# Performance work log

Measured on AMD Instinct MI355X. Metric: run time of the kernel, lower is better.

The kernel has to match this reference:

```python
import jax, jax.numpy as jnp
import numpy as np

IN_DIM = 1024
BS, NCROPS = 32, 1024


def setup_inputs() -> dict:
    key = jax.random.key(0)
    ks = jax.random.split(key, 7)
    s = 1.0 / np.sqrt(IN_DIM)
    return {
        "x": jax.random.normal(ks[0], (BS, NCROPS, IN_DIM), jnp.float32),
        "Wq": jax.random.uniform(ks[1], (IN_DIM,), jnp.float32, -s, s),
        "bq": jax.random.uniform(ks[2], (1,), jnp.float32, -s, s),
        "Wk": jax.random.uniform(ks[3], (IN_DIM,), jnp.float32, -s, s),
        "bk": jax.random.uniform(ks[4], (1,), jnp.float32, -s, s),
        "Wv": jax.random.uniform(ks[5], (IN_DIM, IN_DIM), jnp.float32, -s, s),
        "bv": jax.random.uniform(ks[6], (IN_DIM,), jnp.float32, -s, s),
    }


def reference(x, Wq, bq, Wk, bk, Wv, bv):
    # x: (bs, n, d). 1x1 Conv1d over permuted x == per-position linear maps.
    bs, n, d = x.shape
    q = jnp.einsum("bnd,d->bn", x, Wq) + bq  # (bs, n)   query_conv -> 1 channel
    k = jnp.einsum("bnd,d->bn", x, Wk) + bk  # (bs, n)   key_conv   -> 1 channel
    energy = q[:, :, None] * k[:, None, :]    # (bs, n, n) rank-1 outer product (bmm of (n,1)@(1,n))
    attention = jax.nn.softmax(energy, axis=-1)
    v = jnp.einsum("od,bnd->bon", Wv, x) + bv[None, :, None]  # (bs, d, n) value_conv
    out = jnp.einsum("bdn,bnm->bdm", v, attention)            # (bs, d, n)
    # Faithful to torch .view: raw reshape of (bs, d, n) -> (bs, n, d), NOT a transpose.
    out = out.reshape(bs, n, d)
    return (out, attention)
```

## Files before the change

### kernel.cpp

```cpp
#include <hip/hip_runtime.h>
#include <hip/hip_bf16.h>

#define BS  32
#define N   1024
#define DIM 1024

typedef unsigned short u16;
typedef unsigned int   u32;

typedef __attribute__((ext_vector_type(8))) __bf16 bf16x8;
typedef __attribute__((ext_vector_type(4))) float  f32x4;

__device__ __forceinline__ u16 f2bf(float f) {
    u32 u = __builtin_bit_cast(u32, f);
    u = (u + 0x7FFF + ((u >> 16) & 1)) >> 16;
    return (u16)u;
}

__device__ __forceinline__ void async16(const u16* g, u16* l) {
    __builtin_amdgcn_global_load_lds(
        (const __attribute__((address_space(1))) u32*)g,
        (__attribute__((address_space(3))) u32*)l,
        16, 0, 0);
}

__global__ void convert_qk(const float* __restrict__ x,
                           const float* __restrict__ Wq, const float* __restrict__ bq,
                           const float* __restrict__ Wk, const float* __restrict__ bk,
                           const float* __restrict__ Wv,
                           u16* __restrict__ xb, u16* __restrict__ Wvb,
                           float* __restrict__ qv, float* __restrict__ kv)
{
    int gw   = (blockIdx.x * 256 + threadIdx.x) >> 6;
    int lane = threadIdx.x & 63;
    bool isX = gw < BS * N;
    const float* src = isX ? (x + (size_t)gw * DIM) : (Wv + (size_t)(gw - BS * N) * DIM);
    u16*         dst = isX ? (xb + (size_t)gw * DIM) : (Wvb + (size_t)(gw - BS * N) * DIM);
    float qd = 0.f, kd = 0.f;
    #pragma unroll
    for (int i = 0; i < 4; ++i) {
        int e = i * 256 + lane * 4;
        float4 xv = *(const float4*)&src[e];
        uint2 p;
        p.x = (u32)f2bf(xv.x) | ((u32)f2bf(xv.y) << 16);
        p.y = (u32)f2bf(xv.z) | ((u32)f2bf(xv.w) << 16);
        *(uint2*)&dst[e] = p;
        if (isX) {
            float4 wq = *(const float4*)&Wq[e];
            float4 wk = *(const float4*)&Wk[e];
            qd += xv.x * wq.x + xv.y * wq.y + xv.z * wq.z + xv.w * wq.w;
            kd += xv.x * wk.x + xv.y * wk.y + xv.z * wk.z + xv.w * wk.w;
        }
    }
    if (isX) {
        #pragma unroll
        for (int off = 32; off; off >>= 1) {
            qd += __shfl_xor(qd, off);
            kd += __shfl_xor(kd, off);
        }
        if (lane == 0) { qv[gw] = qd + bq[0]; kv[gw] = kd + bk[0]; }
    }
}

__global__ void qz_writer(const float* __restrict__ qv, const float* __restrict__ kvg,
                          float2* __restrict__ qzg)
{
    int blk = blockIdx.x;
    int b   = blk >> 6;
    int r0  = (blk & 63) * 16;
    __shared__ float ks[1024];
    int tid = threadIdx.x;
    #pragma unroll
    for (int i = 0; i < 4; ++i) ks[i * 256 + tid] = kvg[b * N + i * 256 + tid];
    int row = tid >> 4;
    int c16 = tid & 15;
    float qrow = qv[b * N + r0 + row];
    __syncthreads();
    float z = 0.f;
    #pragma unroll 4
    for (int s = 0; s < 16; ++s) {
        const float4 kk = *(const float4*)&ks[(c16 + s * 16) * 4];
        z += __expf(qrow * kk.x) + __expf(qrow * kk.y)
           + __expf(qrow * kk.z) + __expf(qrow * kk.w);
    }
    z += __shfl_xor(z, 1); z += __shfl_xor(z, 2);
    z += __shfl_xor(z, 4); z += __shfl_xor(z, 8);
    if (c16 == 0) qzg[b * N + r0 + row] = make_float2(qrow, 1.0f / z);
}

__global__ void att_tiles(const float2* __restrict__ qzg, const float* __restrict__ kvg,
                          float* __restrict__ att, u16* __restrict__ attT)
{
    int blk  = blockIdx.x;
    int b    = blk >> 8;
    int rest = blk & 255;
    int r0 = (rest >> 4) * 64;
    int c0 = (rest & 15) * 64;
    int tid = threadIdx.x;
    int tx = tid & 15, ty = tid >> 4;

    float q[4], iz[4];
    #pragma unroll
    for (int i = 0; i < 4; ++i) {
        float2 p = qzg[(size_t)b * N + r0 + tx * 4 + i];
        q[i] = p.x; iz[i] = p.y;
    }
    float kvj[4];
    #pragma unroll
    for (int j = 0; j < 4; ++j) kvj[j] = kvg[(size_t)b * N + c0 + ty * 4 + j];

    float e[4][4];
    #pragma unroll
    for (int i = 0; i < 4; ++i)
        #pragma unroll
        for (int j = 0; j < 4; ++j)
            e[i][j] = __expf(q[i] * kvj[j]) * iz[i];

    float* ab = att + (size_t)b * N * N;
    #pragma unroll
    for (int i = 0; i < 4; ++i) {
        float4 o = make_float4(e[i][0], e[i][1], e[i][2], e[i][3]);
        *(float4*)&ab[(size_t)(r0 + tx * 4 + i) * N + c0 + ty * 4] = o;
    }
    u16* tb = attT + (size_t)b * N * N;
    #pragma unroll
    for (int j = 0; j < 4; ++j) {
        uint2 p;
        p.x = (u32)f2bf(e[0][j]) | ((u32)f2bf(e[1][j]) << 16);
        p.y = (u32)f2bf(e[2][j]) | ((u32)f2bf(e[3][j]) << 16);
        *(uint2*)&tb[(size_t)(c0 + ty * 4 + j) * N + r0 + tx * 4] = p;
    }
}

__global__ __launch_bounds__(256) void gemm_bt(
    const u16* __restrict__ A,
    const u16* __restrict__ B, size_t bBatch,
    u16* __restrict__ C, size_t cBatch,
    const float* __restrict__ bias)
{
    const int K = 1024, LD = 1024;
    int blk  = blockIdx.x;
    int rest = blk >> 3;
    int b    = (blk & 7) * 4 + (rest >> 6);
    int t    = rest & 63;
    int m0  = (t >> 3) * 128, n0 = (t & 7) * 128;
    const u16* Ab = A;
    const u16* Bb = B + bBatch * (size_t)b;
    __shared__ u16 lA[128 * 32];
    __shared__ u16 lB[128 * 32];
    int w = threadIdx.x >> 6, lane = threadIdx.x & 63;
    int wr = (w >> 1) * 64, wc = (w & 1) * 64;
    int rowl = lane >> 2;
    int col8 = (lane & 3) * 8;
    int frow = lane & 15, fk = (lane >> 4) * 8;
    f32x4 acc[4][4] = {};

    for (int k0 = 0; k0 < K; k0 += 32) {
        #pragma unroll
        for (int s = 0; s < 2; ++s) {
            int rr = (s * 4 + w) * 16;
            async16(Ab + (size_t)(m0 + rr + rowl) * LD + k0 + col8, &lA[rr * 32]);
            async16(Bb + (size_t)(n0 + rr + rowl) * LD + k0 + col8, &lB[rr * 32]);
        }
        __syncthreads();
        bf16x8 af[4], bfr[4];
        #pragma unroll
        for (int i = 0; i < 4; ++i)
            af[i] = *(const bf16x8*)&lA[(wr + i * 16 + frow) * 32 + fk];
        #pragma unroll
        for (int j = 0; j < 4; ++j)
            bfr[j] = *(const bf16x8*)&lB[(wc + j * 16 + frow) * 32 + fk];
        #pragma unroll
        for (int i = 0; i < 4; ++i)
            #pragma unroll
            for (int j = 0; j < 4; ++j)
                acc[i][j] = __builtin_amdgcn_mfma_f32_16x16x32_bf16(af[i], bfr[j], acc[i][j], 0, 0, 0);
        __syncthreads();
    }

    int r4 = (lane >> 4) * 4, cc = lane & 15;
    u16* Cb = C + cBatch * (size_t)b;
    #pragma unroll
    for (int i = 0; i < 4; ++i)
        #pragma unroll
        for (int j = 0; j < 4; ++j)
            #pragma unroll
            for (int rg = 0; rg < 4; ++rg) {
                int row = m0 + wr + i * 16 + r4 + rg;
                int col = n0 + wc + j * 16 + cc;
                Cb[(size_t)row * LD + col] = f2bf(acc[i][j][rg] + bias[row]);
            }
}

__global__ __launch_bounds__(256) void gemm2_bt(
    const u16* __restrict__ A, size_t aBatch,
    const u16* __restrict__ B, size_t bBatch,
    float* __restrict__ C, size_t cBatch)
{
    const int K = 1024, LD = 1024;
    int blk  = blockIdx.x;
    int rest = blk >> 3;
    int b    = (blk & 7) * 4 + (rest >> 6);
    int t    = rest & 63;
    int m0  = (t >> 3) * 128, n0 = (t & 7) * 128;
    const u16* Ab = A + aBatch * (size_t)b;
    const u16* Bb = B + bBatch * (size_t)b;
    __shared__ u16 lA[128 * 32];
    __shared__ u16 lB[128 * 32];
    int w = threadIdx.x >> 6, lane = threadIdx.x & 63;
    int wr = (w >> 1) * 64, wc = (w & 1) * 64;
    int rowl = lane >> 2;
    int col8 = (lane & 3) * 8;
    int frow = lane & 15, fk = (lane >> 4) * 8;
    f32x4 acc[4][4] = {};

    for (int k0 = 0; k0 < K; k0 += 32) {
        #pragma unroll
        for (int s = 0; s < 2; ++s) {
            int rr = (s * 4 + w) * 16;
            async16(Ab + (size_t)(m0 + rr + rowl) * LD + k0 + col8, &lA[rr * 32]);
            async16(Bb + (size_t)(n0 + rr + rowl) * LD + k0 + col8, &lB[rr * 32]);
        }
        __syncthreads();
        bf16x8 af[4], bfr[4];
        #pragma unroll
        for (int i = 0; i < 4; ++i)
            af[i] = *(const bf16x8*)&lA[(wr + i * 16 + frow) * 32 + fk];
        #pragma unroll
        for (int j = 0; j < 4; ++j)
            bfr[j] = *(const bf16x8*)&lB[(wc + j * 16 + frow) * 32 + fk];
        #pragma unroll
        for (int i = 0; i < 4; ++i)
            #pragma unroll
            for (int j = 0; j < 4; ++j)
                acc[i][j] = __builtin_amdgcn_mfma_f32_16x16x32_bf16(af[i], bfr[j], acc[i][j], 0, 0, 0);
        __syncthreads();
    }

    int r4 = (lane >> 4) * 4, cc = lane & 15;
    float* Cb = C + cBatch * (size_t)b;
    #pragma unroll
    for (int i = 0; i < 4; ++i)
        #pragma unroll
        for (int j = 0; j < 4; ++j)
            #pragma unroll
            for (int rg = 0; rg < 4; ++rg) {
                int row = m0 + wr + i * 16 + r4 + rg;
                int col = n0 + wc + j * 16 + cc;
                Cb[(size_t)row * LD + col] = acc[i][j][rg];
            }
}

extern "C" void kernel_launch(void* const* d_in, const int* in_sizes, int n_in,
                              void* d_out, int out_size, void* d_ws, size_t ws_size,
                              hipStream_t stream)
{
    const float* x  = (const float*)d_in[0];
    const float* Wq = (const float*)d_in[1];
    const float* bq = (const float*)d_in[2];
    const float* Wk = (const float*)d_in[3];
    const float* bk = (const float*)d_in[4];
    const float* Wv = (const float*)d_in[5];
    const float* bv = (const float*)d_in[6];

    float* out = (float*)d_out;
    float* att = out + (size_t)BS * N * N;

    char* ws = (char*)d_ws;
    u16*  xb   = (u16*)ws;
    u16*  vb   = xb + (size_t)BS * N * DIM;
    u16*  Wvb  = vb + (size_t)BS * N * DIM;
    float* qv  = (float*)(Wvb + (size_t)DIM * DIM);
    float* kv  = qv + BS * N;
    float2* qzg = (float2*)(kv + BS * N);
    u16*  attT = (u16*)(qzg + BS * N);

    convert_qk<<<(BS * N + DIM) / 4, 256, 0, stream>>>(x, Wq, bq, Wk, bk, Wv, xb, Wvb, qv, kv);
    qz_writer<<<BS * 64, 256, 0, stream>>>(qv, kv, qzg);
    gemm_bt<<<BS * 64, 256, 0, stream>>>(Wvb, xb, (size_t)N * DIM, vb, (size_t)N * DIM, bv);
    att_tiles<<<BS * 256, 256, 0, stream>>>(qzg, kv, att, attT);
    gemm2_bt<<<BS * 64, 256, 0, stream>>>(vb, (size_t)N * DIM, attT, (size_t)N * N, out, (size_t)N * DIM);
}
```

Measured before the change: 609.1 us.

## Replace both GEMMs with 256x256-tile, 8-wave, double-buffered swizzled-LDS MFMA kernel

The two simple 128x128 bf16 GEMM kernels, which synchronize on every K-step, are replaced by one templated kernel. It uses 256x256 output tiles, 512 threads, a 128KB double-buffered LDS ring with XOR-swizzled rows, and 64-wide K tiles. Global-to-LDS async loads are issued in quarter-tile chunks interleaved with the MFMA phases, with explicit vmcnt/lgkmcnt waits and s_setprio. The aim is to hide load latency, cut LDS bank conflicts and raise per-block arithmetic intensity. The cost is heavy register and LDS pressure (at most one block per CU with 128KB of LDS) and fragile hand-placed wait counts.

Result: faster. 524.6 us, median of 2 (-13.9%).

```diff
diff --git a/kernel.cpp b/kernel.cpp
--- a/kernel.cpp
+++ b/kernel.cpp
@@ -15,13 +15,6 @@
     u32 u = __builtin_bit_cast(u32, f);
     u = (u + 0x7FFF + ((u >> 16) & 1)) >> 16;
     return (u16)u;
-}
-
-__device__ __forceinline__ void async16(const u16* g, u16* l) {
-    __builtin_amdgcn_global_load_lds(
-        (const __attribute__((address_space(1))) u32*)g,
-        (__attribute__((address_space(3))) u32*)l,
-        16, 0, 0);
 }
 
 __global__ void convert_qk(const float* __restrict__ x,
@@ -132,123 +125,149 @@
     }
 }
 
-__global__ __launch_bounds__(256) void gemm_bt(
-    const u16* __restrict__ A,
-    const u16* __restrict__ B, size_t bBatch,
-    u16* __restrict__ C, size_t cBatch,
-    const float* __restrict__ bias)
-{
-    const int K = 1024, LD = 1024;
-    int blk  = blockIdx.x;
-    int rest = blk >> 3;
-    int b    = (blk & 7) * 4 + (rest >> 6);
-    int t    = rest & 63;
-    int m0  = (t >> 3) * 128, n0 = (t & 7) * 128;
-    const u16* Ab = A;
-    const u16* Bb = B + bBatch * (size_t)b;
-    __shared__ u16 lA[128 * 32];
-    __shared__ u16 lB[128 * 32];
-    int w = threadIdx.x >> 6, lane = threadIdx.x & 63;
-    int wr = (w >> 1) * 64, wc = (w & 1) * 64;
-    int rowl = lane >> 2;
-    int col8 = (lane & 3) * 8;
-    int frow = lane & 15, fk = (lane >> 4) * 8;
-    f32x4 acc[4][4] = {};
-
-    for (int k0 = 0; k0 < K; k0 += 32) {
-        #pragma unroll
-        for (int s = 0; s < 2; ++s) {
-            int rr = (s * 4 + w) * 16;
-            async16(Ab + (size_t)(m0 + rr + rowl) * LD + k0 + col8, &lA[rr * 32]);
-            async16(Bb + (size_t)(n0 + rr + rowl) * LD + k0 + col8, &lB[rr * 32]);
-        }
-        __syncthreads();
-        bf16x8 af[4], bfr[4];
-        #pragma unroll
-        for (int i = 0; i < 4; ++i)
-            af[i] = *(const bf16x8*)&lA[(wr + i * 16 + frow) * 32 + fk];
-        #pragma unroll
-        for (int j = 0; j < 4; ++j)
-            bfr[j] = *(const bf16x8*)&lB[(wc + j * 16 + frow) * 32 + fk];
-        #pragma unroll
-        for (int i = 0; i < 4; ++i)
-            #pragma unroll
-            for (int j = 0; j < 4; ++j)
-                acc[i][j] = __builtin_amdgcn_mfma_f32_16x16x32_bf16(af[i], bfr[j], acc[i][j], 0, 0, 0);
-        __syncthreads();
-    }
-
-    int r4 = (lane >> 4) * 4, cc = lane & 15;
-    u16* Cb = C + cBatch * (size_t)b;
-    #pragma unroll
-    for (int i = 0; i < 4; ++i)
-        #pragma unroll
-        for (int j = 0; j < 4; ++j)
-            #pragma unroll
-            for (int rg = 0; rg < 4; ++rg) {
-                int row = m0 + wr + i * 16 + r4 + rg;
-                int col = n0 + wc + j * 16 + cc;
-                Cb[(size_t)row * LD + col] = f2bf(acc[i][j][rg] + bias[row]);
-            }
-}
-
-__global__ __launch_bounds__(256) void gemm2_bt(
+
+__device__ __forceinline__ void stage_half8(const u16* __restrict__ Aptr,
+                                            const u16* __restrict__ Bptr,
+                                            int m0b, int n0b, char* smem,
+                                            int h, int w, int lane)
+{
+    if (h >= 64) return;
+    int tile = h >> 2, id = h & 3;
+    int db   = tile & 1;
+    const u16* G = (id < 2) ? Bptr : Aptr;
+    int opb   = (id < 2) ? 65536 : 0;
+    int row0  = (id < 2) ? n0b : m0b;
+    int halfb = (id & 1) * 16384;
+    int kb    = tile * 128;
+    int cb    = ((lane & 7) ^ (lane >> 3)) << 4;
+    #pragma unroll
+    for (int i = 0; i < 2; ++i) {
+        int lofs = opb + db * 32768 + halfb + (i * 8 + w) * 1024;
+        int r    = (id & 1) * 128 + (i * 8 + w) * 8 + (lane >> 3);
+        const char* src = (const char*)G + (size_t)(row0 + r) * 2048 + kb + cb;
+        __builtin_amdgcn_global_load_lds(
+            (const __attribute__((address_space(1))) u32*)src,
+            (__attribute__((address_space(3))) u32*)(smem + lofs), 16, 0, 0);
+    }
+}
+
+template<bool BF16OUT>
+__global__ __launch_bounds__(512, 2) void gemm8p(
     const u16* __restrict__ A, size_t aBatch,
     const u16* __restrict__ B, size_t bBatch,
-    float* __restrict__ C, size_t cBatch)
-{
-    const int K = 1024, LD = 1024;
-    int blk  = blockIdx.x;
-    int rest = blk >> 3;
-    int b    = (blk & 7) * 4 + (rest >> 6);
-    int t    = rest & 63;
-    int m0  = (t >> 3) * 128, n0 = (t & 7) * 128;
-    const u16* Ab = A + aBatch * (size_t)b;
-    const u16* Bb = B + bBatch * (size_t)b;
-    __shared__ u16 lA[128 * 32];
-    __shared__ u16 lB[128 * 32];
-    int w = threadIdx.x >> 6, lane = threadIdx.x & 63;
-    int wr = (w >> 1) * 64, wc = (w & 1) * 64;
-    int rowl = lane >> 2;
-    int col8 = (lane & 3) * 8;
-    int frow = lane & 15, fk = (lane >> 4) * 8;
-    f32x4 acc[4][4] = {};
-
-    for (int k0 = 0; k0 < K; k0 += 32) {
+    void* __restrict__ Cv, size_t cBatch,
+    const float* __restrict__ bias)
+{
+    __shared__ char smem[131072];
+    int bid = blockIdx.x;
+    int lin = (bid & 7) * 64 + (bid >> 3);
+    int b   = lin >> 4;
+    int t16 = lin & 15;
+    int m0b = (t16 >> 2) * 256, n0b = (t16 & 3) * 256;
+    const u16* Aptr = A + aBatch * (size_t)b;
+    const u16* Bptr = B + bBatch * (size_t)b;
+
+    int tid  = threadIdx.x;
+    int w    = tid >> 6, lane = tid & 63;
+    int wm   = w >> 2, wn = w & 3;
+
+    f32x4 acc[8][4] = {};
+    bf16x8 aP[2][2], aQ[2][2], bF[4][2];
+
+#define LDA_(dst, fi, ks) dst = *(const bf16x8*)(smem + jdb * 32768 + \
+        (wm * 128 + (fi) * 16 + (lane & 15)) * 128 + \
+        ((((ks) * 64) + ((lane >> 4) << 4)) ^ ((lane & 7) << 4)))
+#define LDB_(dst, ni, ks) dst = *(const bf16x8*)(smem + 65536 + jdb * 32768 + \
+        (wn * 64 + (ni) * 16 + (lane & 15)) * 128 + \
+        ((((ks) * 64) + ((lane >> 4) << 4)) ^ ((lane & 7) << 4)))
+#define MFMA_HALF(FI0, AR) do { \
+        __builtin_amdgcn_s_setprio(1); \
+        _Pragma("unroll") \
+        for (int mi = 0; mi < 2; ++mi) \
+            _Pragma("unroll") \
+            for (int ni = 0; ni < 4; ++ni) \
+                _Pragma("unroll") \
+                for (int ks = 0; ks < 2; ++ks) \
+                    acc[(FI0) + mi][ni] = __builtin_amdgcn_mfma_f32_16x16x32_bf16( \
+                        AR[mi][ks], bF[ni][ks], acc[(FI0) + mi][ni], 0, 0, 0); \
+        __builtin_amdgcn_s_setprio(0); \
+    } while (0)
+
+    #pragma unroll
+    for (int h = 0; h < 7; ++h) stage_half8(Aptr, Bptr, m0b, n0b, smem, h, w, lane);
+    asm volatile("s_waitcnt vmcnt(6)" ::: "memory");
+    __builtin_amdgcn_s_barrier();
+    __builtin_amdgcn_sched_barrier(0);
+
+    #pragma unroll 1
+    for (int j = 0; j < 16; ++j) {
+        const int jdb = j & 1;
+        LDA_(aP[0][0], 0, 0); LDA_(aP[0][1], 0, 1);
+        LDA_(aP[1][0], 1, 0); LDA_(aP[1][1], 1, 1);
+        LDA_(aQ[0][0], 2, 0); LDA_(aQ[0][1], 2, 1);
+        LDA_(aQ[1][0], 3, 0); LDA_(aQ[1][1], 3, 1);
+        LDB_(bF[0][0], 0, 0); LDB_(bF[0][1], 0, 1);
+        LDB_(bF[1][0], 1, 0); LDB_(bF[1][1], 1, 1);
+        LDB_(bF[2][0], 2, 0); LDB_(bF[2][1], 2, 1);
+        LDB_(bF[3][0], 3, 0); LDB_(bF[3][1], 3, 1);
+        stage_half8(Aptr, Bptr, m0b, n0b, smem, 7 + 4 * j, w, lane);
+        __builtin_amdgcn_s_barrier();
+        asm volatile("s_waitcnt lgkmcnt(0)" ::: "memory");
+        MFMA_HALF(0, aP);
+        __builtin_amdgcn_s_barrier();
+        LDA_(aP[0][0], 4, 0); LDA_(aP[0][1], 4, 1);
+        LDA_(aP[1][0], 5, 0); LDA_(aP[1][1], 5, 1);
+        stage_half8(Aptr, Bptr, m0b, n0b, smem, 8 + 4 * j, w, lane);
+        __builtin_amdgcn_s_barrier();
+        asm volatile("s_waitcnt lgkmcnt(0)" ::: "memory");
+        MFMA_HALF(2, aQ);
+        __builtin_amdgcn_s_barrier();
+        LDA_(aQ[0][0], 6, 0); LDA_(aQ[0][1], 6, 1);
+        LDA_(aQ[1][0], 7, 0); LDA_(aQ[1][1], 7, 1);
+        stage_half8(Aptr, Bptr, m0b, n0b, smem, 9 + 4 * j, w, lane);
+        __builtin_amdgcn_s_barrier();
+        asm volatile("s_waitcnt lgkmcnt(0)" ::: "memory");
+        MFMA_HALF(4, aP);
+        __builtin_amdgcn_s_barrier();
+        stage_half8(Aptr, Bptr, m0b, n0b, smem, 10 + 4 * j, w, lane);
+        __builtin_amdgcn_s_barrier();
+        asm volatile("s_waitcnt lgkmcnt(0)" ::: "memory");
+        MFMA_HALF(6, aQ);
+        if (j < 14)       asm volatile("s_waitcnt vmcnt(6)" ::: "memory");
+        else if (j == 14) asm volatile("s_waitcnt vmcnt(0)" ::: "memory");
+        __builtin_amdgcn_s_barrier();
+        __builtin_amdgcn_sched_barrier(0);
+    }
+#undef LDA_
+#undef LDB_
+#undef MFMA_HALF
+
+    int r4 = (lane >> 4) * 4, cc = lane & 15;
+    if constexpr (BF16OUT) {
+        u16* Cb = (u16*)Cv + cBatch * (size_t)b;
         #pragma unroll
-        for (int s = 0; s < 2; ++s) {
-            int rr = (s * 4 + w) * 16;
-            async16(Ab + (size_t)(m0 + rr + rowl) * LD + k0 + col8, &lA[rr * 32]);
-            async16(Bb + (size_t)(n0 + rr + rowl) * LD + k0 + col8, &lB[rr * 32]);
-        }
-        __syncthreads();
-        bf16x8 af[4], bfr[4];
+        for (int fi = 0; fi < 8; ++fi)
+            #pragma unroll
+            for (int ni = 0; ni < 4; ++ni)
+                #pragma unroll
+                for (int rg = 0; rg < 4; ++rg) {
+                    int row = m0b + wm * 128 + fi * 16 + r4 + rg;
+                    int col = n0b + wn * 64 + ni * 16 + cc;
+                    Cb[(size_t)row * 1024 + col] = f2bf(acc[fi][ni][rg] + bias[row]);
+                }
+    } else {
+        float* Cb = (float*)Cv + cBatch * (size_t)b;
         #pragma unroll
-        for (int i = 0; i < 4; ++i)
-            af[i] = *(const bf16x8*)&lA[(wr + i * 16 + frow) * 32 + fk];
-        #pragma unroll
-        for (int j = 0; j < 4; ++j)
-            bfr[j] = *(const bf16x8*)&lB[(wc + j * 16 + frow) * 32 + fk];
-        #pragma unroll
-        for (int i = 0; i < 4; ++i)
+        for (int fi = 0; fi < 8; ++fi)
             #pragma unroll
-            for (int j = 0; j < 4; ++j)
-                acc[i][j] = __builtin_amdgcn_mfma_f32_16x16x32_bf16(af[i], bfr[j], acc[i][j], 0, 0, 0);
-        __syncthreads();
-    }
-
-    int r4 = (lane >> 4) * 4, cc = lane & 15;
-    float* Cb = C + cBatch * (size_t)b;
-    #pragma unroll
-    for (int i = 0; i < 4; ++i)
-        #pragma unroll
-        for (int j = 0; j < 4; ++j)
-            #pragma unroll
-            for (int rg = 0; rg < 4; ++rg) {
-                int row = m0 + wr + i * 16 + r4 + rg;
-                int col = n0 + wc + j * 16 + cc;
-                Cb[(size_t)row * LD + col] = acc[i][j][rg];
-            }
+            for (int ni = 0; ni < 4; ++ni)
+                #pragma unroll
+                for (int rg = 0; rg < 4; ++rg) {
+                    int row = m0b + wm * 128 + fi * 16 + r4 + rg;
+                    int col = n0b + wn * 64 + ni * 16 + cc;
+                    Cb[(size_t)row * 1024 + col] = acc[fi][ni][rg];
+                }
+    }
 }
 
 extern "C" void kernel_launch(void* const* d_in, const int* in_sizes, int n_in,
@@ -277,7 +296,7 @@
 
     convert_qk<<<(BS * N + DIM) / 4, 256, 0, stream>>>(x, Wq, bq, Wk, bk, Wv, xb, Wvb, qv, kv);
     qz_writer<<<BS * 64, 256, 0, stream>>>(qv, kv, qzg);
-    gemm_bt<<<BS * 64, 256, 0, stream>>>(Wvb, xb, (size_t)N * DIM, vb, (size_t)N * DIM, bv);
+    gemm8p<true><<<512, 512, 0, stream>>>(Wvb, 0, xb, (size_t)N * DIM, vb, (size_t)N * DIM, bv);
     att_tiles<<<BS * 256, 256, 0, stream>>>(qzg, kv, att, attT);
-    gemm2_bt<<<BS * 64, 256, 0, stream>>>(vb, (size_t)N * DIM, attT, (size_t)N * N, out, (size_t)N * DIM);
-}
+    gemm8p<false><<<512, 512, 0, stream>>>(vb, (size_t)N * DIM, attT, (size_t)N * N, out, (size_t)N * DIM, nullptr);
+}
```
